# Kernel tuning notes

Measured on AMD Instinct MI355X. Metric: run time of the kernel, lower is better.

## Reference

```python
import jax, jax.numpy as jnp
import numpy as np

N_NODES = 50000
N_EDGES = 800000
NUM_GRAPHS = 128
KS = 5           # kernel_size per pseudo dim
K = KS * KS      # 25 spline weight matrices per layer


def spline_coeff(pseudo):
    """Open linear (degree-1) B-spline basis for 2-D pseudo coords in [0,1].
    Returns dense per-edge coefficients over the K=25 kernel slots: [E, K]."""
    pos = pseudo * (KS - 1)                      # [E,2]
    lo = jnp.clip(jnp.floor(pos).astype(jnp.int32), 0, KS - 2)
    frac = pos - lo.astype(pseudo.dtype)         # [E,2]
    i0, i1 = lo, lo + 1
    w0, w1 = 1.0 - frac, frac
    # 2^dim = 4 corner combinations, flat index = d0 + KS*d1
    idx = jnp.stack([i0[:, 0] + KS * i0[:, 1],
                     i0[:, 0] + KS * i1[:, 1],
                     i1[:, 0] + KS * i0[:, 1],
                     i1[:, 0] + KS * i1[:, 1]], axis=1)            # [E,4]
    w = jnp.stack([w0[:, 0] * w0[:, 1], w0[:, 0] * w1[:, 1],
                   w1[:, 0] * w0[:, 1], w1[:, 0] * w1[:, 1]], axis=1)  # [E,4]
    E = pseudo.shape[0]
    coeff = jnp.zeros((E, K), pseudo.dtype).at[jnp.arange(E)[:, None], idx].add(w)
    return coeff


def spline_conv(x, coeff, src, dst, W, root, bias):
    """SplineConv: gather src feats, spline-weighted transform, scatter-mean to dst,
    plus root weight and bias. x:[N,in], coeff:[E,K], W:[K,in,out]."""
    n = x.shape[0]
    x_src = x[src]                                # [E,in] gather
    m = coeff[:, 0:1] * (x_src @ W[0])            # [E,out]
    for k in range(1, K):                         # fixed small loop over K kernels
        m = m + coeff[:, k:k + 1] * (x_src @ W[k])
    agg = jax.ops.segment_sum(m, dst, num_segments=n)
    cnt = jax.ops.segment_sum(jnp.ones((src.shape[0],), x.dtype), dst, num_segments=n)
    agg = agg / jnp.maximum(cnt, 1.0)[:, None]    # mean aggregation (PyG default)
    return agg + x @ root + bias


def setup_inputs() -> dict:
    key = jax.random.key(0)
    ks = jax.random.split(key, 16)
    s = 0.1  # small init scale for numerical stability
    return {
        "x": jax.random.normal(ks[0], (N_NODES, 1), jnp.float32),
        "position": jax.random.uniform(ks[1], (N_NODES, 2), jnp.float32),
        "pseudo": jax.random.uniform(ks[2], (N_EDGES, 2), jnp.float32),
        "edge_index": jax.random.randint(ks[3], (2, N_EDGES), 0, N_NODES, jnp.int32),
        "batch": jnp.sort(jax.random.randint(ks[4], (N_NODES,), 0, NUM_GRAPHS, jnp.int32)),
        "W1": s * jax.random.normal(ks[5], (K, 1, 32), jnp.float32),
        "root1": s * jax.random.normal(ks[6], (1, 32), jnp.float32),
        "b1": jnp.zeros((32,), jnp.float32),
        "W2": s * jax.random.normal(ks[7], (K, 32, 64), jnp.float32),
        "root2": s * jax.random.normal(ks[8], (32, 64), jnp.float32),
        "b2": jnp.zeros((64,), jnp.float32),
        "W3": s * jax.random.normal(ks[9], (K, 64, 64), jnp.float32),
        "root3": s * jax.random.normal(ks[10], (64, 64), jnp.float32),
        "b3": jnp.zeros((64,), jnp.float32),
        "fc_w": s * jax.random.normal(ks[11], (64, 10), jnp.float32),
        "fc_b": jnp.zeros((10,), jnp.float32),
    }


def reference(x, position, pseudo, edge_index, batch,
              W1, root1, b1, W2, root2, b2, W3, root3, b3, fc_w, fc_b):
    # `position` is accepted but unused, matching the original forward.
    src, dst = edge_index[0], edge_index[1]
    coeff = spline_coeff(pseudo)
    h = jax.nn.elu(spline_conv(x, coeff, src, dst, W1, root1, b1))
    h = jax.nn.elu(spline_conv(h, coeff, src, dst, W2, root2, b2))
    h = jax.nn.elu(spline_conv(h, coeff, src, dst, W3, root3, b3))
    # scatter_mean pooling over batch indices -> [NUM_GRAPHS, 64]
    pooled = jax.ops.segment_sum(h, batch, num_segments=NUM_GRAPHS)
    gcnt = jax.ops.segment_sum(jnp.ones((h.shape[0],), h.dtype), batch,
                               num_segments=NUM_GRAPHS)
    pooled = pooled / jnp.maximum(gcnt, 1.0)[:, None]
    # dropout is identity in eval mode
    logits = pooled @ fc_w + fc_b
    return jax.nn.log_softmax(logits, axis=1)
```

## Files before the change

kernel.cpp:

```cpp
#include <hip/hip_runtime.h>

#define NN 50000
#define NE 800000
#define NG 128
#define NB_SCAN 196

typedef unsigned int uint;
typedef unsigned short ushort;
typedef __attribute__((ext_vector_type(8))) short short8;
typedef __attribute__((ext_vector_type(4))) float f32x4;
typedef __attribute__((ext_vector_type(16))) float f32x16;

__device__ __forceinline__ float bf2f(ushort u){ union{uint i; float f;} v; v.i=(uint)u<<16; return v.f; }
__device__ __forceinline__ ushort f2bf(float f){ union{float f; uint i;} v; v.f=f; return (ushort)((v.i + 0x7FFFu + ((v.i>>16)&1u))>>16); }

__global__ void zero_k(int* hist, float* pooled, int* gcnt){
    int i = blockIdx.x*blockDim.x + threadIdx.x;
    if (i < NN) hist[i] = 0;
    if (i < NG*64) pooled[i] = 0.f;
    if (i < NG) gcnt[i] = 0;
}

__global__ void hist_k(const int* __restrict__ ei, int* __restrict__ hist){
    int e = blockIdx.x*blockDim.x + threadIdx.x;
    if (e < NE) atomicAdd(&hist[ei[NE + e]], 1);
}

__global__ __launch_bounds__(256) void scan1(const int* __restrict__ hist, int* __restrict__ bsum){
    __shared__ int sm[256];
    int t = threadIdx.x, i = blockIdx.x*256 + t;
    sm[t] = (i < NN) ? hist[i] : 0;
    __syncthreads();
    for (int o = 128; o > 0; o >>= 1){ if (t < o) sm[t] += sm[t+o]; __syncthreads(); }
    if (t == 0) bsum[blockIdx.x] = sm[0];
}
__global__ __launch_bounds__(256) void scan2(const int* __restrict__ bsum, int* __restrict__ bpre){
    __shared__ int sm[256];
    int t = threadIdx.x;
    int v = (t < NB_SCAN) ? bsum[t] : 0;
    sm[t] = v; __syncthreads();
    int acc = v;
    for (int o = 1; o < 256; o <<= 1){
        int u = (t >= o) ? sm[t-o] : 0; __syncthreads();
        acc += u; sm[t] = acc; __syncthreads();
    }
    if (t < NB_SCAN) bpre[t] = acc - v;
}
__global__ __launch_bounds__(256) void scan3(const int* __restrict__ hist, const int* __restrict__ bpre,
                                             int* __restrict__ offs, int* __restrict__ cursor,
                                             float* __restrict__ invc){
    __shared__ int sm[256];
    int t = threadIdx.x, b = blockIdx.x, i = b*256 + t;
    int v = (i < NN) ? hist[i] : 0;
    sm[t] = v; __syncthreads();
    int acc = v;
    for (int o = 1; o < 256; o <<= 1){
        int u = (t >= o) ? sm[t-o] : 0; __syncthreads();
        acc += u; sm[t] = acc; __syncthreads();
    }
    int excl = acc - v + bpre[b];
    if (i < NN){ offs[i] = excl; cursor[i] = excl; invc[i] = 1.0f/(float)max(v,1); }
    if (i == NN-1) offs[NN] = NE;
}

__global__ void scatter_k(const int* __restrict__ ei, const float* __restrict__ pseudo,
                          int* __restrict__ cursor, uint4* __restrict__ payload2){
    int e = blockIdx.x*blockDim.x + threadIdx.x;
    if (e >= NE) return;
    float2 ps = *(const float2*)(pseudo + 2*(size_t)e);
    float px = ps.x * 4.0f, py = ps.y * 4.0f;
    int lx = min(max((int)floorf(px), 0), 3);
    int ly = min(max((int)floorf(py), 0), 3);
    float fx = px - (float)lx, fy = py - (float)ly;
    float gx = 1.f - fx, gy = 1.f - fy;
    float w00 = gx*gy, w10 = fx*gy, w01 = gx*fy, w11 = fx*fy;
    ushort h00 = f2bf(w00), h10 = f2bf(w10), h01 = f2bf(w01), h11 = f2bf(w11);
    ushort L00 = f2bf(w00 - bf2f(h00)), L10 = f2bf(w10 - bf2f(h10));
    ushort L01 = f2bf(w01 - bf2f(h01)), L11 = f2bf(w11 - bf2f(h11));
    uint meta = (uint)ei[e] | ((uint)lx<<16) | ((uint)ly<<18);
    int pos = atomicAdd(&cursor[ei[NE + e]], 1);
    payload2[(size_t)pos*2]   = make_uint4(meta, (uint)h00 | ((uint)h10<<16),
                                                 (uint)h01 | ((uint)h11<<16),
                                                 (uint)L00 | ((uint)L10<<16));
    payload2[(size_t)pos*2+1] = make_uint4((uint)L01 | ((uint)L11<<16), 0u, 0u, 0u);
}

template<int IN>
__global__ void wprep_k(const float* __restrict__ W, const float* __restrict__ root, ushort* __restrict__ Bp){
    const int total = 26*IN*64;
    int tid = blockIdx.x*blockDim.x + threadIdx.x;
    if (tid >= total) return;
    int j    = tid & 7;
    int lane = (tid >> 3) & 63;
    int ctkt = tid >> 9;
    int ct   = ctkt & 3;
    int kt   = ctkt >> 2;
    int kk   = kt*32 + (lane>>4)*8 + j;
    int col  = ct*16 + (lane & 15);
    float v;
    if (kk < 25*IN){ int k = kk / IN; int i = kk % IN; v = W[((size_t)k*IN + i)*64 + col]; }
    else           { v = root[(size_t)(kk - 25*IN)*64 + col]; }
    Bp[tid] = f2bf(v);
}

__global__ __launch_bounds__(256) void reduce1_k(const float* __restrict__ x, const uint4* __restrict__ payload2,
                                                 const int* __restrict__ offs, const float* __restrict__ invc,
                                                 const float* __restrict__ W1, const float* __restrict__ root1,
                                                 const float* __restrict__ b1, ushort* __restrict__ h1bf){
    __shared__ float w1s[25*32];
    for (int i = threadIdx.x; i < 25*32; i += 256) w1s[i] = W1[i];
    __syncthreads();
    int wid  = threadIdx.x >> 6;
    int lane = threadIdx.x & 63;
    int o    = lane & 31;
    int half = lane >> 5;
    int d    = blockIdx.x*4 + wid;
    int s = offs[d], e = offs[d+1];
    float acc = 0.f;
    for (int p = s; p < e; ++p){
        uint4 q0 = payload2[(size_t)p*2];
        uint lo23 = payload2[(size_t)p*2+1].x;
        uint meta = q0.x;
        int lx = (meta>>16)&3, ly = (meta>>18)&3;
        float wa, wb;
        if (half == 0){ wa = bf2f((ushort)q0.y) + bf2f((ushort)q0.w);
                        wb = bf2f((ushort)q0.z) + bf2f((ushort)lo23); }
        else          { wa = bf2f((ushort)(q0.y>>16)) + bf2f((ushort)(q0.w>>16));
                        wb = bf2f((ushort)(q0.z>>16)) + bf2f((ushort)(lo23>>16)); }
        float xs = x[meta & 0xFFFF];
        int ka = ly*5 + lx + half;
        acc += (wa*w1s[ka*32 + o] + wb*w1s[(ka+5)*32 + o]) * xs;
    }
    acc += __shfl_xor(acc, 32);
    if (half == 0){
        float val = acc*invc[d] + x[d]*root1[o] + b1[o];
        val = val > 0.f ? val : expm1f(val);
        h1bf[(size_t)d*32 + o] = f2bf(val);
    }
}

template<int IN, int MODE>
__global__ __launch_bounds__(512) void fused_mf3(
        const ushort* __restrict__ hin, const uint4* __restrict__ payload2,
        const int* __restrict__ offs, const float* __restrict__ invc,
        const ushort* __restrict__ Bp, const float* __restrict__ bias,
        const int* __restrict__ batch, ushort* __restrict__ hout,
        float* __restrict__ pooled, int* __restrict__ gcnt)
{
    constexpr int NCT = IN/32;
    constexpr int KT  = 26*IN/32, KH = KT/2;
    __shared__ __align__(16) ushort Sb[KT*512];
    __shared__ __align__(16) uint4 estage[8][32];
    __shared__ float red[1024];
    __shared__ float outS[1024];

    const int tid = threadIdx.x, lane = tid & 63, w = tid >> 6;
    const int ln31 = lane & 31, kg2 = lane >> 5;
    const int d0 = blockIdx.x * 16;
    const int i0 = ln31 % 5, j0 = ln31 / 5;
    const bool rv = (ln31 < 25);

    for (int nn = 0; nn < 2; ++nn){
        const int node = w*2 + nn;
        const int d = d0 + node;
        int s = offs[d];
        int h = offs[d+1] - s;
        int steps = (h + 15) >> 4;

        f32x16 accH[NCT];
        #pragma unroll
        for (int ct = 0; ct < NCT; ++ct)
            #pragma unroll
            for (int q = 0; q < 16; ++q) accH[ct][q] = 0.f;

        for (int ks = 0; ks < steps; ++ks){
            int rem2 = (h - ks*16)*2;
            if (lane < 32){
                uint4 v = make_uint4(0u,0u,0u,0u);
                if (lane < rem2) v = payload2[(size_t)(s + ks*16)*2 + lane];
                estage[w][lane] = v;
            }
            short8 ah, al;
            uint srcs[8];
            #pragma unroll
            for (int j = 0; j < 8; ++j){
                int es = kg2*8 + j;
                uint4 q0  = estage[w][es*2];
                uint lo23 = estage[w][es*2+1].x;
                uint meta = q0.x;
                int lx = (meta>>16)&3, ly = (meta>>18)&3;
                int dx = i0 - lx, dy = j0 - ly;
                bool ok = rv && ((uint)dx < 2u) && ((uint)dy < 2u);
                uint hiw = (dy == 1) ? q0.z : q0.y;
                uint low = (dy == 1) ? lo23 : q0.w;
                int sh = (dx & 1) << 4;
                ah[j] = ok ? (short)((hiw >> sh) & 0xFFFFu) : (short)0;
                al[j] = ok ? (short)((low >> sh) & 0xFFFFu) : (short)0;
                srcs[j] = meta & 0xFFFFu;
            }
            short8 bfv[NCT];
            #pragma unroll
            for (int j = 0; j < 8; ++j){
                const ushort* hb = hin + (size_t)srcs[j]*IN + ln31;
                #pragma unroll
                for (int ct = 0; ct < NCT; ++ct)
                    bfv[ct][j] = (short)hb[ct*32];
            }
            #pragma unroll
            for (int ct = 0; ct < NCT; ++ct){
                accH[ct] = __builtin_amdgcn_mfma_f32_32x32x16_bf16(ah, bfv[ct], accH[ct], 0, 0, 0);
                accH[ct] = __builtin_amdgcn_mfma_f32_32x32x16_bf16(al, bfv[ct], accH[ct], 0, 0, 0);
            }
        }

        {
            float ic = invc[d];
            int jd  = ln31 & 7;
            int l3  = ln31 >> 3;
            #pragma unroll
            for (int reg = 0; reg < 16; ++reg){
                int r = (reg & 3) + 8*(reg >> 2) + 4*kg2;
                if (r < 25){
                    #pragma unroll
                    for (int ct = 0; ct < NCT; ++ct){
                        int kt  = r*NCT + ct;
                        int kgt = (ct*4 + l3) & 3;
                        Sb[kt*512 + kgt*128 + node*8 + jd] = f2bf(accH[ct][reg]*ic);
                    }
                }
            }
            if (IN == 64){
                int f = lane;
                Sb[(25*NCT + (f>>5))*512 + ((f>>3)&3)*128 + node*8 + (f&7)] = hin[(size_t)d*64 + f];
            } else if (lane < 32){
                int f = lane;
                Sb[25*512 + ((f>>3)&3)*128 + node*8 + (f&7)] = hin[(size_t)d*32 + f];
            }
        }
    }
    __syncthreads();

    {
        int ct = w & 3, kh = w >> 2;
        int c15 = lane & 15, kg = lane >> 4;
        f32x4 a4 = {0.f,0.f,0.f,0.f};
        const ushort* bb = Bp + ct*512 + (size_t)lane*8;
        #pragma unroll
        for (int k = 0; k < KH; ++k){
            int kt = kh*KH + k;
            short8 a = *(const short8*)(Sb + kt*512 + lane*8);
            short8 b = *(const short8*)(bb + (size_t)kt*2048);
            a4 = __builtin_amdgcn_mfma_f32_16x16x32_bf16(a, b, a4, 0, 0, 0);
        }
        if (kh == 1){
            float* rr = red + (ct*64 + lane)*4;
            rr[0]=a4[0]; rr[1]=a4[1]; rr[2]=a4[2]; rr[3]=a4[3];
        }
        __syncthreads();
        if (kh == 0){
            const float* rr = red + (ct*64 + lane)*4;
            int col = ct*16 + c15;
            float bs = bias[col];
            #pragma unroll
            for (int jq = 0; jq < 4; ++jq){
                int r16 = kg*4 + jq;
                float v = a4[jq] + rr[jq] + bs;
                v = v > 0.f ? v : expm1f(v);
                if (MODE == 0) ((ushort*)outS)[r16*64 + col] = f2bf(v);
                else           outS[r16*64 + col] = v;
            }
        }
    }
    __syncthreads();

    if (MODE == 0){
        uint* dst = (uint*)(hout + (size_t)d0*64);
        const uint* srcp = (const uint*)outS;
        dst[tid] = srcp[tid];
    } else {
        if (w == 0){
            int c = lane;
            float run = 0.f; int gprev = batch[d0];
            for (int r = 0; r < 16; ++r){
                int g = batch[d0 + r];
                if (g != gprev){ atomicAdd(&pooled[gprev*64 + c], run); run = 0.f; gprev = g; }
                run += outS[r*64 + c];
            }
            atomicAdd(&pooled[gprev*64 + c], run);
        } else if (w == 1 && lane == 0){
            int cnt = 0; int gprev = batch[d0];
            for (int r = 0; r < 16; ++r){
                int g = batch[d0 + r];
                if (g != gprev){ atomicAdd(&gcnt[gprev], cnt); cnt = 0; gprev = g; }
                cnt++;
            }
            atomicAdd(&gcnt[gprev], cnt);
        }
    }
}

__global__ __launch_bounds__(128) void head_k(const float* __restrict__ pooled, const int* __restrict__ gcnt,
                                              const float* __restrict__ fcw, const float* __restrict__ fcb,
                                              float* __restrict__ out){
    int g = threadIdx.x;
    if (g >= NG) return;
    float inv = 1.0f / fmaxf((float)gcnt[g], 1.0f);
    float logits[10];
    #pragma unroll
    for (int c = 0; c < 10; ++c) logits[c] = fcb[c];
    for (int o = 0; o < 64; ++o){
        float m = pooled[g*64 + o] * inv;
        #pragma unroll
        for (int c = 0; c < 10; ++c) logits[c] += m * fcw[o*10 + c];
    }
    float mx = logits[0];
    #pragma unroll
    for (int c = 1; c < 10; ++c) mx = fmaxf(mx, logits[c]);
    float ssum = 0.f;
    #pragma unroll
    for (int c = 0; c < 10; ++c) ssum += expf(logits[c] - mx);
    float lse = logf(ssum) + mx;
    #pragma unroll
    for (int c = 0; c < 10; ++c) out[g*10 + c] = logits[c] - lse;
}

extern "C" void kernel_launch(void* const* d_in, const int* in_sizes, int n_in,
                              void* d_out, int out_size, void* d_ws, size_t ws_size,
                              hipStream_t stream) {
    const float* x      = (const float*)d_in[0];
    const float* pseudo = (const float*)d_in[2];
    const int*   ei     = (const int*)  d_in[3];
    const int*   batch  = (const int*)  d_in[4];
    const float* W1     = (const float*)d_in[5];
    const float* root1  = (const float*)d_in[6];
    const float* b1     = (const float*)d_in[7];
    const float* W2     = (const float*)d_in[8];
    const float* root2  = (const float*)d_in[9];
    const float* b2     = (const float*)d_in[10];
    const float* W3     = (const float*)d_in[11];
    const float* root3  = (const float*)d_in[12];
    const float* b3     = (const float*)d_in[13];
    const float* fcw    = (const float*)d_in[14];
    const float* fcb    = (const float*)d_in[15];
    float* out = (float*)d_out;

    char* ws = (char*)d_ws;
    size_t off = 0;
    auto alloc = [&](size_t bytes)->char*{ char* p = ws + off; off += (bytes + 255) / 256 * 256; return p; };
    uint4*  payload2= (uint4*)alloc((size_t)NE*32);
    ushort* h1bf   = (ushort*)alloc((size_t)NN*32*2);
    ushort* h2bf   = (ushort*)alloc((size_t)NN*64*2);
    int*    hist   = (int*)   alloc((size_t)NN*4);
    int*    offs   = (int*)   alloc((size_t)(NN+1)*4);
    int*    cursor = (int*)   alloc((size_t)NN*4);
    float*  invc   = (float*) alloc((size_t)NN*4);
    int*    bsum   = (int*)   alloc((size_t)NB_SCAN*4);
    int*    bpre   = (int*)   alloc((size_t)NB_SCAN*4);
    ushort* Bp2    = (ushort*)alloc((size_t)26*2048*2);
    ushort* Bp3    = (ushort*)alloc((size_t)52*2048*2);
    float*  pooled = (float*) alloc((size_t)NG*64*4);
    int*    gcnt   = (int*)   alloc((size_t)NG*4);
    (void)ws_size; (void)in_sizes; (void)n_in; (void)out_size;

    zero_k   <<<NB_SCAN, 256, 0, stream>>>(hist, pooled, gcnt);
    hist_k   <<<(NE+255)/256, 256, 0, stream>>>(ei, hist);
    scan1    <<<NB_SCAN, 256, 0, stream>>>(hist, bsum);
    scan2    <<<1, 256, 0, stream>>>(bsum, bpre);
    scan3    <<<NB_SCAN, 256, 0, stream>>>(hist, bpre, offs, cursor, invc);
    scatter_k<<<(NE+255)/256, 256, 0, stream>>>(ei, pseudo, cursor, payload2);
    wprep_k<32><<<(26*32*64 + 255)/256, 256, 0, stream>>>(W2, root2, Bp2);
    wprep_k<64><<<(26*64*64 + 255)/256, 256, 0, stream>>>(W3, root3, Bp3);
    reduce1_k<<<NN/4, 256, 0, stream>>>(x, payload2, offs, invc, W1, root1, b1, h1bf);
    fused_mf3<32,0><<<NN/16, 512, 0, stream>>>(h1bf, payload2, offs, invc, Bp2, b2, batch, h2bf, pooled, gcnt);
    fused_mf3<64,1><<<NN/16, 512, 0, stream>>>(h2bf, payload2, offs, invc, Bp3, b3, batch, h2bf, pooled, gcnt);
    head_k   <<<1, 128, 0, stream>>>(pooled, gcnt, fcw, fcb, out);
}
```

Baseline: 330.3 us.

## Use 1024-thread blocks with one node per wave, prefetch edges, swizzle LDS

Each block keeps 16 nodes but now launches 16 waves, one node per wave, where before 8 waves each handled two nodes in sequence. The second-stage GEMM splits the K range across 4 wave groups and reduces their partial sums in shared memory. Payload for the next edge chunk is loaded into registers one step ahead, and the staged LDS tile uses an XOR swizzle to cut bank conflicts. This trades more per-block threads and register pressure (launch_bounds 1024) for more parallelism and latency hiding.

```diff
diff --git a/kernel.cpp b/kernel.cpp
--- a/kernel.cpp
+++ b/kernel.cpp
@@ -13,6 +13,7 @@
 
 __device__ __forceinline__ float bf2f(ushort u){ union{uint i; float f;} v; v.i=(uint)u<<16; return v.f; }
 __device__ __forceinline__ ushort f2bf(float f){ union{float f; uint i;} v; v.f=f; return (ushort)((v.i + 0x7FFFu + ((v.i>>16)&1u))>>16); }
+__device__ __forceinline__ int iswz(int i){ return i ^ ((i>>4)&3); }
 
 __global__ void zero_k(int* hist, float* pooled, int* gcnt){
     int i = blockIdx.x*blockDim.x + threadIdx.x;
@@ -140,7 +141,7 @@
 }
 
 template<int IN, int MODE>
-__global__ __launch_bounds__(512) void fused_mf3(
+__global__ __launch_bounds__(1024, 8) void fused_mf4(
         const ushort* __restrict__ hin, const uint4* __restrict__ payload2,
         const int* __restrict__ offs, const float* __restrict__ invc,
         const ushort* __restrict__ Bp, const float* __restrict__ bias,
@@ -148,10 +149,10 @@
         float* __restrict__ pooled, int* __restrict__ gcnt)
 {
     constexpr int NCT = IN/32;
-    constexpr int KT  = 26*IN/32, KH = KT/2;
+    constexpr int KT  = 26*IN/32;
     __shared__ __align__(16) ushort Sb[KT*512];
-    __shared__ __align__(16) uint4 estage[8][32];
-    __shared__ float red[1024];
+    __shared__ __align__(16) uint4 estage[16][32];
+    __shared__ __align__(16) float red[3*4*256];
     __shared__ float outS[1024];
 
     const int tid = threadIdx.x, lane = tid & 63, w = tid >> 6;
@@ -160,9 +161,8 @@
     const int i0 = ln31 % 5, j0 = ln31 / 5;
     const bool rv = (ln31 < 25);
 
-    for (int nn = 0; nn < 2; ++nn){
-        const int node = w*2 + nn;
-        const int d = d0 + node;
+    {
+        const int d = d0 + w;
         int s = offs[d];
         int h = offs[d+1] - s;
         int steps = (h + 15) >> 4;
@@ -173,12 +173,18 @@
             #pragma unroll
             for (int q = 0; q < 16; ++q) accH[ct][q] = 0.f;
 
+        uint4 v = make_uint4(0u,0u,0u,0u);
+        {
+            int rem2 = h*2; if (rem2 > 32) rem2 = 32;
+            if (lane < rem2) v = payload2[(size_t)s*2 + lane];
+        }
         for (int ks = 0; ks < steps; ++ks){
-            int rem2 = (h - ks*16)*2;
-            if (lane < 32){
-                uint4 v = make_uint4(0u,0u,0u,0u);
-                if (lane < rem2) v = payload2[(size_t)(s + ks*16)*2 + lane];
-                estage[w][lane] = v;
+            if (lane < 32) estage[w][lane] = v;
+            if (ks+1 < steps){
+                int rem2 = (h - (ks+1)*16)*2; if (rem2 > 32) rem2 = 32;
+                uint4 nv = make_uint4(0u,0u,0u,0u);
+                if (lane < rem2) nv = payload2[(size_t)(s + (ks+1)*16)*2 + lane];
+                v = nv;
             }
             short8 ah, al;
             uint srcs[8];
@@ -215,26 +221,27 @@
 
         {
             float ic = invc[d];
-            int jd  = ln31 & 7;
-            int l3  = ln31 >> 3;
+            int jd = ln31 & 7;
+            int l3 = ln31 >> 3;
+            int ig = iswz(l3*16 + w);
             #pragma unroll
             for (int reg = 0; reg < 16; ++reg){
                 int r = (reg & 3) + 8*(reg >> 2) + 4*kg2;
                 if (r < 25){
                     #pragma unroll
-                    for (int ct = 0; ct < NCT; ++ct){
-                        int kt  = r*NCT + ct;
-                        int kgt = (ct*4 + l3) & 3;
-                        Sb[kt*512 + kgt*128 + node*8 + jd] = f2bf(accH[ct][reg]*ic);
-                    }
+                    for (int ct = 0; ct < NCT; ++ct)
+                        Sb[(r*NCT + ct)*512 + ig*8 + jd] = f2bf(accH[ct][reg]*ic);
                 }
             }
             if (IN == 64){
                 int f = lane;
-                Sb[(25*NCT + (f>>5))*512 + ((f>>3)&3)*128 + node*8 + (f&7)] = hin[(size_t)d*64 + f];
+                int kt = 25*NCT + (f>>5);
+                int ig2 = iswz(((f>>3)&3)*16 + w);
+                Sb[kt*512 + ig2*8 + (f&7)] = hin[(size_t)d*64 + f];
             } else if (lane < 32){
                 int f = lane;
-                Sb[25*512 + ((f>>3)&3)*128 + node*8 + (f&7)] = hin[(size_t)d*32 + f];
+                int ig2 = iswz(((f>>3)&3)*16 + w);
+                Sb[25*512 + ig2*8 + (f&7)] = hin[(size_t)d*32 + f];
             }
         }
     }
@@ -242,41 +249,47 @@
 
     {
         int ct = w & 3, kh = w >> 2;
-        int c15 = lane & 15, kg = lane >> 4;
+        const int KH4 = KT/4, rem = KT & 3;
+        int kbeg = kh*KH4 + min(kh, rem);
+        int kcnt = KH4 + (kh < rem ? 1 : 0);
+        int ig = iswz(lane);
         f32x4 a4 = {0.f,0.f,0.f,0.f};
         const ushort* bb = Bp + ct*512 + (size_t)lane*8;
-        #pragma unroll
-        for (int k = 0; k < KH; ++k){
-            int kt = kh*KH + k;
-            short8 a = *(const short8*)(Sb + kt*512 + lane*8);
+        for (int k = 0; k < kcnt; ++k){
+            int kt = kbeg + k;
+            short8 a = *(const short8*)(Sb + kt*512 + ig*8);
             short8 b = *(const short8*)(bb + (size_t)kt*2048);
             a4 = __builtin_amdgcn_mfma_f32_16x16x32_bf16(a, b, a4, 0, 0, 0);
         }
-        if (kh == 1){
-            float* rr = red + (ct*64 + lane)*4;
-            rr[0]=a4[0]; rr[1]=a4[1]; rr[2]=a4[2]; rr[3]=a4[3];
-        }
+        if (kh > 0)
+            *(f32x4*)&red[(((kh-1)*4 + ct)*64 + lane)*4] = a4;
         __syncthreads();
         if (kh == 0){
-            const float* rr = red + (ct*64 + lane)*4;
+            #pragma unroll
+            for (int q = 0; q < 3; ++q){
+                f32x4 rr = *(const f32x4*)&red[((q*4 + ct)*64 + lane)*4];
+                a4[0] += rr[0]; a4[1] += rr[1]; a4[2] += rr[2]; a4[3] += rr[3];
+            }
+            int c15 = lane & 15, kg = lane >> 4;
             int col = ct*16 + c15;
             float bs = bias[col];
             #pragma unroll
             for (int jq = 0; jq < 4; ++jq){
                 int r16 = kg*4 + jq;
-                float v = a4[jq] + rr[jq] + bs;
-                v = v > 0.f ? v : expm1f(v);
-                if (MODE == 0) ((ushort*)outS)[r16*64 + col] = f2bf(v);
-                else           outS[r16*64 + col] = v;
+                float vv = a4[jq] + bs;
+                vv = vv > 0.f ? vv : expm1f(vv);
+                if (MODE == 0) ((ushort*)outS)[r16*64 + col] = f2bf(vv);
+                else           outS[r16*64 + col] = vv;
             }
         }
     }
     __syncthreads();
 
     if (MODE == 0){
-        uint* dst = (uint*)(hout + (size_t)d0*64);
-        const uint* srcp = (const uint*)outS;
-        dst[tid] = srcp[tid];
+        if (tid < 512){
+            uint* dst = (uint*)(hout + (size_t)d0*64);
+            dst[tid] = ((const uint*)outS)[tid];
+        }
     } else {
         if (w == 0){
             int c = lane;
@@ -371,7 +384,7 @@
     wprep_k<32><<<(26*32*64 + 255)/256, 256, 0, stream>>>(W2, root2, Bp2);
     wprep_k<64><<<(26*64*64 + 255)/256, 256, 0, stream>>>(W3, root3, Bp3);
     reduce1_k<<<NN/4, 256, 0, stream>>>(x, payload2, offs, invc, W1, root1, b1, h1bf);
-    fused_mf3<32,0><<<NN/16, 512, 0, stream>>>(h1bf, payload2, offs, invc, Bp2, b2, batch, h2bf, pooled, gcnt);
-    fused_mf3<64,1><<<NN/16, 512, 0, stream>>>(h2bf, payload2, offs, invc, Bp3, b3, batch, h2bf, pooled, gcnt);
+    fused_mf4<32,0><<<NN/16, 1024, 0, stream>>>(h1bf, payload2, offs, invc, Bp2, b2, batch, h2bf, pooled, gcnt);
+    fused_mf4<64,1><<<NN/16, 1024, 0, stream>>>(h2bf, payload2, offs, invc, Bp3, b3, batch, h2bf, pooled, gcnt);
     head_k   <<<1, 128, 0, stream>>>(pooled, gcnt, fcw, fcb, out);
 }
```

After: 406.3 us. +23.0%, slower.

## Split edge payload into 16B+4B arrays, prefetch next chunk, swizzle LDS A tiles

Applied to the files above, without the earlier changes.

Replaces the padded 32-byte per-edge payload with a 16-byte array plus a separate 4-byte array, cutting the payload bytes written and read by each of the three layers. The edge staging loop in the fused MFMA kernel now prefetches the next 16-edge chunk into registers while the current one is processed. It also applies an XOR swizzle to the LDS A-operand layout to reduce bank conflicts on writes and MFMA loads. In exchange the kernel uses more registers and does extra index arithmetic, and the payload reads are split into two separate loads.

```diff
diff --git a/kernel.cpp b/kernel.cpp
--- a/kernel.cpp
+++ b/kernel.cpp
@@ -13,6 +13,7 @@
 
 __device__ __forceinline__ float bf2f(ushort u){ union{uint i; float f;} v; v.i=(uint)u<<16; return v.f; }
 __device__ __forceinline__ ushort f2bf(float f){ union{float f; uint i;} v; v.f=f; return (ushort)((v.i + 0x7FFFu + ((v.i>>16)&1u))>>16); }
+__device__ __forceinline__ int iswz(int i){ return i ^ ((i>>4)&3); }
 
 __global__ void zero_k(int* hist, float* pooled, int* gcnt){
     int i = blockIdx.x*blockDim.x + threadIdx.x;
@@ -64,7 +65,7 @@
 }
 
 __global__ void scatter_k(const int* __restrict__ ei, const float* __restrict__ pseudo,
-                          int* __restrict__ cursor, uint4* __restrict__ payload2){
+                          int* __restrict__ cursor, uint4* __restrict__ payA, uint* __restrict__ payB){
     int e = blockIdx.x*blockDim.x + threadIdx.x;
     if (e >= NE) return;
     float2 ps = *(const float2*)(pseudo + 2*(size_t)e);
@@ -79,10 +80,10 @@
     ushort L01 = f2bf(w01 - bf2f(h01)), L11 = f2bf(w11 - bf2f(h11));
     uint meta = (uint)ei[e] | ((uint)lx<<16) | ((uint)ly<<18);
     int pos = atomicAdd(&cursor[ei[NE + e]], 1);
-    payload2[(size_t)pos*2]   = make_uint4(meta, (uint)h00 | ((uint)h10<<16),
-                                                 (uint)h01 | ((uint)h11<<16),
-                                                 (uint)L00 | ((uint)L10<<16));
-    payload2[(size_t)pos*2+1] = make_uint4((uint)L01 | ((uint)L11<<16), 0u, 0u, 0u);
+    payA[pos] = make_uint4(meta, (uint)h00 | ((uint)h10<<16),
+                                 (uint)h01 | ((uint)h11<<16),
+                                 (uint)L00 | ((uint)L10<<16));
+    payB[pos] = (uint)L01 | ((uint)L11<<16);
 }
 
 template<int IN>
@@ -103,7 +104,8 @@
     Bp[tid] = f2bf(v);
 }
 
-__global__ __launch_bounds__(256) void reduce1_k(const float* __restrict__ x, const uint4* __restrict__ payload2,
+__global__ __launch_bounds__(256) void reduce1_k(const float* __restrict__ x, const uint4* __restrict__ payA,
+                                                 const uint* __restrict__ payB,
                                                  const int* __restrict__ offs, const float* __restrict__ invc,
                                                  const float* __restrict__ W1, const float* __restrict__ root1,
                                                  const float* __restrict__ b1, ushort* __restrict__ h1bf){
@@ -118,8 +120,8 @@
     int s = offs[d], e = offs[d+1];
     float acc = 0.f;
     for (int p = s; p < e; ++p){
-        uint4 q0 = payload2[(size_t)p*2];
-        uint lo23 = payload2[(size_t)p*2+1].x;
+        uint4 q0 = payA[p];
+        uint lo23 = payB[p];
         uint meta = q0.x;
         int lx = (meta>>16)&3, ly = (meta>>18)&3;
         float wa, wb;
@@ -140,8 +142,8 @@
 }
 
 template<int IN, int MODE>
-__global__ __launch_bounds__(512) void fused_mf3(
-        const ushort* __restrict__ hin, const uint4* __restrict__ payload2,
+__global__ __launch_bounds__(512) void fused_r13(
+        const ushort* __restrict__ hin, const uint4* __restrict__ payA, const uint* __restrict__ payB,
         const int* __restrict__ offs, const float* __restrict__ invc,
         const ushort* __restrict__ Bp, const float* __restrict__ bias,
         const int* __restrict__ batch, ushort* __restrict__ hout,
@@ -150,7 +152,8 @@
     constexpr int NCT = IN/32;
     constexpr int KT  = 26*IN/32, KH = KT/2;
     __shared__ __align__(16) ushort Sb[KT*512];
-    __shared__ __align__(16) uint4 estage[8][32];
+    __shared__ __align__(16) uint4 eA[8][16];
+    __shared__ uint eB[8][16];
     __shared__ float red[1024];
     __shared__ float outS[1024];
 
@@ -173,20 +176,31 @@
             #pragma unroll
             for (int q = 0; q < 16; ++q) accH[ct][q] = 0.f;
 
+        uint4 vA = make_uint4(0u,0u,0u,0u); uint vB = 0u;
+        {
+            int rem = (h < 16) ? h : 16;
+            if (lane < rem) vA = payA[(size_t)s + lane];
+            int j2 = lane - 16;
+            if (j2 >= 0 && j2 < rem) vB = payB[(size_t)s + j2];
+        }
         for (int ks = 0; ks < steps; ++ks){
-            int rem2 = (h - ks*16)*2;
-            if (lane < 32){
-                uint4 v = make_uint4(0u,0u,0u,0u);
-                if (lane < rem2) v = payload2[(size_t)(s + ks*16)*2 + lane];
-                estage[w][lane] = v;
+            if (lane < 16) eA[w][lane] = vA;
+            else if (lane < 32) eB[w][lane-16] = vB;
+            if (ks+1 < steps){
+                int rem = h - (ks+1)*16; if (rem > 16) rem = 16;
+                uint4 nA = make_uint4(0u,0u,0u,0u); uint nB = 0u;
+                if (lane < rem) nA = payA[(size_t)(s + (ks+1)*16) + lane];
+                int j2 = lane - 16;
+                if (j2 >= 0 && j2 < rem) nB = payB[(size_t)(s + (ks+1)*16) + j2];
+                vA = nA; vB = nB;
             }
             short8 ah, al;
             uint srcs[8];
             #pragma unroll
             for (int j = 0; j < 8; ++j){
                 int es = kg2*8 + j;
-                uint4 q0  = estage[w][es*2];
-                uint lo23 = estage[w][es*2+1].x;
+                uint4 q0  = eA[w][es];
+                uint lo23 = eB[w][es];
                 uint meta = q0.x;
                 int lx = (meta>>16)&3, ly = (meta>>18)&3;
                 int dx = i0 - lx, dy = j0 - ly;
@@ -225,16 +239,16 @@
                     for (int ct = 0; ct < NCT; ++ct){
                         int kt  = r*NCT + ct;
                         int kgt = (ct*4 + l3) & 3;
-                        Sb[kt*512 + kgt*128 + node*8 + jd] = f2bf(accH[ct][reg]*ic);
+                        Sb[kt*512 + iswz(kgt*16 + node)*8 + jd] = f2bf(accH[ct][reg]*ic);
                     }
                 }
             }
             if (IN == 64){
                 int f = lane;
-                Sb[(25*NCT + (f>>5))*512 + ((f>>3)&3)*128 + node*8 + (f&7)] = hin[(size_t)d*64 + f];
+                Sb[(25*NCT + (f>>5))*512 + iswz(((f>>3)&3)*16 + node)*8 + (f&7)] = hin[(size_t)d*64 + f];
             } else if (lane < 32){
                 int f = lane;
-                Sb[25*512 + ((f>>3)&3)*128 + node*8 + (f&7)] = hin[(size_t)d*32 + f];
+                Sb[25*512 + iswz(((f>>3)&3)*16 + node)*8 + (f&7)] = hin[(size_t)d*32 + f];
             }
         }
     }
@@ -243,12 +257,13 @@
     {
         int ct = w & 3, kh = w >> 2;
         int c15 = lane & 15, kg = lane >> 4;
+        int ig = iswz(lane);
         f32x4 a4 = {0.f,0.f,0.f,0.f};
         const ushort* bb = Bp + ct*512 + (size_t)lane*8;
         #pragma unroll
         for (int k = 0; k < KH; ++k){
             int kt = kh*KH + k;
-            short8 a = *(const short8*)(Sb + kt*512 + lane*8);
+            short8 a = *(const short8*)(Sb + kt*512 + ig*8);
             short8 b = *(const short8*)(bb + (size_t)kt*2048);
             a4 = __builtin_amdgcn_mfma_f32_16x16x32_bf16(a, b, a4, 0, 0, 0);
         }
@@ -347,7 +362,8 @@
     char* ws = (char*)d_ws;
     size_t off = 0;
     auto alloc = [&](size_t bytes)->char*{ char* p = ws + off; off += (bytes + 255) / 256 * 256; return p; };
-    uint4*  payload2= (uint4*)alloc((size_t)NE*32);
+    uint4*  payA   = (uint4*) alloc((size_t)NE*16);
+    uint*   payB   = (uint*)  alloc((size_t)NE*4);
     ushort* h1bf   = (ushort*)alloc((size_t)NN*32*2);
     ushort* h2bf   = (ushort*)alloc((size_t)NN*64*2);
     int*    hist   = (int*)   alloc((size_t)NN*4);
@@ -367,11 +383,11 @@
     scan1    <<<NB_SCAN, 256, 0, stream>>>(hist, bsum);
     scan2    <<<1, 256, 0, stream>>>(bsum, bpre);
     scan3    <<<NB_SCAN, 256, 0, stream>>>(hist, bpre, offs, cursor, invc);
-    scatter_k<<<(NE+255)/256, 256, 0, stream>>>(ei, pseudo, cursor, payload2);
+    scatter_k<<<(NE+255)/256, 256, 0, stream>>>(ei, pseudo, cursor, payA, payB);
     wprep_k<32><<<(26*32*64 + 255)/256, 256, 0, stream>>>(W2, root2, Bp2);
     wprep_k<64><<<(26*64*64 + 255)/256, 256, 0, stream>>>(W3, root3, Bp3);
-    reduce1_k<<<NN/4, 256, 0, stream>>>(x, payload2, offs, invc, W1, root1, b1, h1bf);
-    fused_mf3<32,0><<<NN/16, 512, 0, stream>>>(h1bf, payload2, offs, invc, Bp2, b2, batch, h2bf, pooled, gcnt);
-    fused_mf3<64,1><<<NN/16, 512, 0, stream>>>(h2bf, payload2, offs, invc, Bp3, b3, batch, h2bf, pooled, gcnt);
+    reduce1_k<<<NN/4, 256, 0, stream>>>(x, payA, payB, offs, invc, W1, root1, b1, h1bf);
+    fused_r13<32,0><<<NN/16, 512, 0, stream>>>(h1bf, payA, payB, offs, invc, Bp2, b2, batch, h2bf, pooled, gcnt);
+    fused_r13<64,1><<<NN/16, 512, 0, stream>>>(h2bf, payA, payB, offs, invc, Bp3, b3, batch, h2bf, pooled, gcnt);
     head_k   <<<1, 128, 0, stream>>>(pooled, gcnt, fcw, fcb, out);
 }
```

New measurement: 314.5 us. 1.05x faster.
